# Kernel tuning notes

Measured on AMD Instinct MI355X. Metric: run time of the kernel, lower is better.

Reference implementation:

```python
import jax, jax.numpy as jnp
import numpy as np

N_CODE, PC = 127, 63
LENGTH = N_CODE + PC          # 190
D_MODEL, D_STATE, D_CONV, EXPAND = 512, 16, 4, 2
D_INNER = EXPAND * D_MODEL    # 1024
DT_RANK = (D_MODEL + 15) // 16  # 32
BATCH = 16


def _build_mask(pcm):
    # faithful translation of build_mask(code)
    L = N_CODE + PC
    mask = np.eye(L, dtype=np.float64)
    for r in range(PC):
        idx = np.where(pcm[r] > 0)[0]
        for jj in idx:
            for kk in idx:
                if jj != kk:
                    mask[jj, kk] += 1
                    mask[kk, jj] += 1
                    mask[N_CODE + r, jj] += 1
                    mask[jj, N_CODE + r] += 1
    return mask > 0


def setup_inputs() -> dict:
    rng = np.random.default_rng(0)
    # LDPC-like sparse parity-check matrix, row weight 6
    pcm = np.zeros((PC, N_CODE), np.int32)
    for r in range(PC):
        pcm[r, rng.choice(N_CODE, 6, replace=False)] = 1
    pc_mask = jnp.asarray(_build_mask(pcm))

    def w(shape, fan_in):
        return jnp.asarray((rng.standard_normal(shape) / np.sqrt(fan_in)).astype(np.float32))

    inp = {
        "x": jnp.asarray(rng.standard_normal((BATCH, LENGTH, D_MODEL)).astype(np.float32)),
        "pc_mask": pc_mask,
        # masked resize linears (torch Linear: y = x @ W.T + b)
        "in_resize_w": w((LENGTH, D_MODEL), D_MODEL),
        "in_resize_b": jnp.zeros((LENGTH,), jnp.float32),
        "in_reset_w": w((D_MODEL, LENGTH), LENGTH),
        "in_reset_b": jnp.zeros((D_MODEL,), jnp.float32),
        "out_resize_w": w((LENGTH, D_MODEL), D_MODEL),
        "out_resize_b": jnp.zeros((LENGTH,), jnp.float32),
        "out_reset_w": w((D_MODEL, LENGTH), LENGTH),
        "out_reset_b": jnp.zeros((D_MODEL,), jnp.float32),
        # Mamba block params
        "in_proj_w": w((2 * D_INNER, D_MODEL), D_MODEL),
        "conv_w": w((D_INNER, D_CONV), D_CONV),          # depthwise conv kernels
        "conv_b": jnp.zeros((D_INNER,), jnp.float32),
        "x_proj_w": w((DT_RANK + 2 * D_STATE, D_INNER), D_INNER),
        "dt_proj_w": w((D_INNER, DT_RANK), DT_RANK),
        "dt_proj_b": jnp.full((D_INNER,), -4.6, jnp.float32),  # softplus ~ 0.01
        "A_log": jnp.log(jnp.tile(jnp.arange(1, D_STATE + 1, dtype=jnp.float32), (D_INNER, 1))),
        "D": jnp.ones((D_INNER,), jnp.float32),
        "out_proj_w": w((D_MODEL, D_INNER), D_INNER),
        # LayerNorm over (length, d_model)
        "norm_w": jnp.ones((LENGTH, D_MODEL), jnp.float32),
        "norm_b": jnp.zeros((LENGTH, D_MODEL), jnp.float32),
    }
    return inp


def _forward(x, pc_mask, in_resize_w, in_resize_b, in_reset_w, in_reset_b,
             out_resize_w, out_resize_b, out_reset_w, out_reset_b,
             in_proj_w, conv_w, conv_b, x_proj_w, dt_proj_w, dt_proj_b,
             A_log, D, out_proj_w, norm_w, norm_b):
    dt_rank = dt_proj_w.shape[1]
    d_state = A_log.shape[1]
    d_conv = conv_w.shape[1]

    def mamba(h):
        # h: [B, L, d_model]
        xz = h @ in_proj_w.T                       # [B, L, 2*d_inner]
        xc, z = jnp.split(xz, 2, axis=-1)
        # depthwise causal conv along L
        xt = xc.transpose(0, 2, 1)                 # [B, d_inner, L]
        xt = jax.lax.conv_general_dilated(
            xt, conv_w[:, None, :], (1,), [(d_conv - 1, 0)],
            dimension_numbers=("NCH", "OIH", "NCH"),
            feature_group_count=xt.shape[1])
        xc = jax.nn.silu((xt + conv_b[None, :, None]).transpose(0, 2, 1))  # [B,L,di]
        x_dbl = xc @ x_proj_w.T                    # [B, L, dt_rank+2*ds]
        dt = jax.nn.softplus(x_dbl[..., :dt_rank] @ dt_proj_w.T + dt_proj_b)
        Bm = x_dbl[..., dt_rank:dt_rank + d_state]  # [B, L, ds]
        Cm = x_dbl[..., dt_rank + d_state:]         # [B, L, ds]
        A = -jnp.exp(A_log)                         # [di, ds]
        dA = jnp.exp(dt[..., None] * A)             # [B, L, di, ds]
        dBu = (dt * xc)[..., None] * Bm[:, :, None, :]

        def step(hst, inp):
            a, b = inp
            hst = a * hst + b
            return hst, hst

        h0 = jnp.zeros((dA.shape[0], dA.shape[2], dA.shape[3]), dA.dtype)
        _, hs = jax.lax.scan(step, h0, (dA.transpose(1, 0, 2, 3), dBu.transpose(1, 0, 2, 3)))
        y = jnp.einsum("lbds,bls->bld", hs, Cm) + xc * D
        return (y * jax.nn.silu(z)) @ out_proj_w.T  # [B, L, d_model]

    m = pc_mask.astype(x.dtype)
    h = (x @ in_resize_w.T + in_resize_b) * m[0, 0]
    h = (h @ in_reset_w.T + in_reset_b) * x
    o = mamba(h) + jnp.flip(mamba(jnp.flip(h, 1)), 1)  # bidirectional scan
    o = (o @ out_resize_w.T + out_resize_b) * m        # [B,L,L] * [L,L]
    o = (o @ out_reset_w.T + out_reset_b) * x
    # LayerNorm over last two dims (length, d_model)
    t = jnp.tanh(x)
    mu = jnp.mean(t, axis=(-2, -1), keepdims=True)
    var = jnp.var(t, axis=(-2, -1), keepdims=True)
    out = (t - mu) * jax.lax.rsqrt(var + 1e-5) * norm_w + norm_b
    # original module returns only `out`; `o` is also returned here to keep the
    # (otherwise dead) bidirectional selective-scan path observable.
    return out, o


def reference(x, pc_mask, in_resize_w, in_resize_b, in_reset_w, in_reset_b,
              out_resize_w, out_resize_b, out_reset_w, out_reset_b,
              in_proj_w, conv_w, conv_b, x_proj_w, dt_proj_w, dt_proj_b,
              A_log, D, out_proj_w, norm_w, norm_b):
    return _forward(x, pc_mask, in_resize_w, in_resize_b, in_reset_w, in_reset_b,
                    out_resize_w, out_resize_b, out_reset_w, out_reset_b,
                    in_proj_w, conv_w, conv_b, x_proj_w, dt_proj_w, dt_proj_b,
                    A_log, D, out_proj_w, norm_w, norm_b)
```

## Files before the change

### kernel.cpp

```cpp
#include <hip/hip_runtime.h>
#include <hip/hip_bf16.h>

#define B_    16
#define L_    190
#define LP_   192
#define DM_   512
#define DI_   1024
#define LB_   3040
#define RT_   6080
#define LBDI_ 3112960

typedef __attribute__((ext_vector_type(8))) short bf16x8;
typedef __attribute__((ext_vector_type(4))) float f32x4;
typedef __attribute__((ext_vector_type(4))) unsigned short u16x4;

typedef const __attribute__((address_space(1))) void gvoid;
typedef __attribute__((address_space(3))) void lvoid;
#define LOAD_LDS16(g, l) __builtin_amdgcn_global_load_lds((gvoid*)(g), (lvoid*)(l), 16, 0, 0)

__device__ __forceinline__ float siluf(float v) { return v / (1.f + __expf(-v)); }
__device__ __forceinline__ float softplusf(float v) {
  return v > 0.f ? v + log1pf(__expf(-v)) : log1pf(__expf(v));
}
__device__ __forceinline__ float bf2f(unsigned short u) {
  unsigned int w = (unsigned int)u << 16; return __builtin_bit_cast(float, w);
}

__global__ __launch_bounds__(256) void mask_convert(const void* __restrict__ pcm,
                                                    float* __restrict__ maskf,
                                                    const float* __restrict__ irb,
                                                    const float* __restrict__ orb,
                                                    float* __restrict__ b_inrs,
                                                    float* __restrict__ b_outrs)
{
  __shared__ int votes[3];
  if (threadIdx.x < 3) votes[threadIdx.x] = 0;
  __syncthreads();
  if (threadIdx.x < 48) {
    int idx = threadIdx.x * 191;
    const unsigned char* p8  = (const unsigned char*)pcm;
    const unsigned int*  p32 = (const unsigned int*)pcm;
    if (p8[idx] == 1) atomicAdd(&votes[0], 1);
    unsigned int v = p32[idx];
    if (v == 1u)          atomicAdd(&votes[1], 1);
    if (v == 0x3f800000u) atomicAdd(&votes[2], 1);
  }
  __syncthreads();
  int mode = (votes[0] >= 48) ? 0 : (votes[1] >= 48 ? 1 : (votes[2] >= 48 ? 2 : 0));
  int i = blockIdx.x * 256 + threadIdx.x;
  if (i < L_ * LP_) {
    int r = i / LP_, c = i % LP_;
    float v = 0.f;
    if (c < L_) {
      int s = r * L_ + c;
      if (mode == 0)      v = ((const unsigned char*)pcm)[s] ? 1.f : 0.f;
      else if (mode == 1) v = ((const int*)pcm)[s] ? 1.f : 0.f;
      else                v = ((const float*)pcm)[s];
    }
    maskf[i] = v;
  }
  if (blockIdx.x == 0 && threadIdx.x < LP_) {
    b_inrs[threadIdx.x]  = (threadIdx.x < L_) ? irb[threadIdx.x] : 0.f;
    b_outrs[threadIdx.x] = (threadIdx.x < L_) ? orb[threadIdx.x] : 0.f;
  }
}

struct Cvt2 { const float* src; __hip_bfloat16* dst; int R, C, Rp, Cp; };
struct CvtPack2 { Cvt2 d[9]; };

__global__ __launch_bounds__(256) void cvt_all2(CvtPack2 p)
{
  Cvt2 D = p.d[blockIdx.y];
  int n = D.Rp * D.Cp;
  if (D.C == D.Cp) {
    int nsrc = D.R * D.C;
    for (int i4 = (blockIdx.x * 256 + threadIdx.x) * 4; i4 < n; i4 += gridDim.x * 256 * 4) {
      __hip_bfloat16 o[4];
      if (i4 + 3 < nsrc) {
        f32x4 v = *(const f32x4*)(D.src + i4);
        #pragma unroll
        for (int q = 0; q < 4; ++q) o[q] = __float2bfloat16(v[q]);
      } else {
        #pragma unroll
        for (int q = 0; q < 4; ++q) { int i = i4 + q; o[q] = __float2bfloat16(i < nsrc ? D.src[i] : 0.f); }
      }
      *(u16x4*)(D.dst + i4) = *(u16x4*)o;
    }
  } else {
    for (int i = blockIdx.x * 256 + threadIdx.x; i < n; i += gridDim.x * 256) {
      int r = i / D.Cp, c = i - r * D.Cp;
      float v = (r < D.R && c < D.C) ? D.src[(size_t)r * D.C + c] : 0.f;
      D.dst[i] = __float2bfloat16(v);
    }
  }
}

template<int EPI, bool OF32, bool OBF>
__global__ __launch_bounds__(256) void gemm128(
    const __hip_bfloat16* __restrict__ A, int lda, int M,
    const __hip_bfloat16* __restrict__ Bw, int Brows,
    const float* __restrict__ bias, const float* __restrict__ aux,
    float* __restrict__ Cf, __hip_bfloat16* __restrict__ Cb,
    int N, int K)
{
  __shared__ bf16x8 SA[2][512];
  __shared__ bf16x8 SB[2][512];
  const int tid = threadIdx.x;
  const int wave = tid >> 6, lane = tid & 63;
  const int m0 = blockIdx.y * 128, n0 = blockIdx.x * 128;
  const int wm = (wave >> 1) * 64, wn = (wave & 1) * 64;
  const int l15 = lane & 15, lkb = lane >> 4;

  f32x4 acc[4][4] = {};

  auto stage = [&](int bsel, int k0) {
    #pragma unroll
    for (int it = 0; it < 2; ++it) {
      int c = it * 256 + tid;
      int row = c & 127, kb = c >> 7;
      int ar = m0 + row; ar = ar < M ? ar : M - 1;
      const __hip_bfloat16* ga = A + (size_t)ar * lda + (k0 + kb * 8);
      LOAD_LDS16(ga, &SA[bsel][it * 256 + wave * 64]);
      int br = n0 + row; br = br < Brows ? br : Brows - 1;
      const __hip_bfloat16* gb = Bw + (size_t)br * K + (k0 + kb * 8);
      LOAD_LDS16(gb, &SB[bsel][it * 256 + wave * 64]);
    }
  };

  const int nk = K >> 5;
  stage(0, 0);
  __syncthreads();
  int buf = 0;
  for (int kt = 0; kt < nk; ++kt) {
    if (kt + 1 < nk) stage(buf ^ 1, (kt + 1) * 32);
    bf16x8 af[4], bq[4];
    #pragma unroll
    for (int f = 0; f < 4; ++f) {
      af[f] = SA[buf][lkb * 128 + wm + f * 16 + l15];
      bq[f] = SB[buf][lkb * 128 + wn + f * 16 + l15];
    }
    #pragma unroll
    for (int i = 0; i < 4; ++i)
      #pragma unroll
      for (int j = 0; j < 4; ++j)
        acc[i][j] = __builtin_amdgcn_mfma_f32_16x16x32_bf16(af[i], bq[j], acc[i][j], 0, 0, 0);
    __syncthreads();
    buf ^= 1;
  }

  #pragma unroll
  for (int i = 0; i < 4; ++i) {
    int r0 = m0 + wm + i * 16 + (lkb << 2);
    #pragma unroll
    for (int j = 0; j < 4; ++j) {
      int col = n0 + wn + j * 16 + l15;
      if (col >= N) continue;
      #pragma unroll
      for (int r = 0; r < 4; ++r) {
        int row = r0 + r;
        if (row >= M) continue;
        float v = acc[i][j][r];
        if (EPI >= 1) v += bias[col];
        if (EPI == 2) v *= aux[(size_t)row * N + col];
        if (EPI == 3) v = softplusf(v);
        if (EPI == 4) v *= aux[(size_t)(row % L_) * N + col];
        if (OF32) Cf[(size_t)row * N + col] = v;
        if (OBF)  Cb[(size_t)row * N + col] = __float2bfloat16(v);
      }
    }
  }
}

template<int EPI, bool OF32, bool OBF>
__global__ __launch_bounds__(256) void gemm64(
    const __hip_bfloat16* __restrict__ A, int lda, int M,
    const __hip_bfloat16* __restrict__ Bw, int Brows,
    const float* __restrict__ bias, const float* __restrict__ aux,
    float* __restrict__ Cf, __hip_bfloat16* __restrict__ Cb,
    int N, int K)
{
  __shared__ bf16x8 SA[2][256];
  __shared__ bf16x8 SB[2][256];
  const int tid = threadIdx.x;
  const int wave = tid >> 6, lane = tid & 63;
  const int m0 = blockIdx.y * 64, n0 = blockIdx.x * 64;
  const int wm = (wave >> 1) * 32, wn = (wave & 1) * 32;
  const int l15 = lane & 15, lkb = lane >> 4;

  f32x4 acc[2][2] = {};

  auto stage = [&](int bsel, int k0) {
    int row = tid & 63, kb = tid >> 6;
    int ar = m0 + row; ar = ar < M ? ar : M - 1;
    const __hip_bfloat16* ga = A + (size_t)ar * lda + (k0 + kb * 8);
    LOAD_LDS16(ga, &SA[bsel][wave * 64]);
    int br = n0 + row; br = br < Brows ? br : Brows - 1;
    const __hip_bfloat16* gb = Bw + (size_t)br * K + (k0 + kb * 8);
    LOAD_LDS16(gb, &SB[bsel][wave * 64]);
  };

  const int nk = K >> 5;
  stage(0, 0);
  __syncthreads();
  int buf = 0;
  for (int kt = 0; kt < nk; ++kt) {
    if (kt + 1 < nk) stage(buf ^ 1, (kt + 1) * 32);
    bf16x8 af[2], bq[2];
    #pragma unroll
    for (int f = 0; f < 2; ++f) {
      af[f] = SA[buf][lkb * 64 + wm + f * 16 + l15];
      bq[f] = SB[buf][lkb * 64 + wn + f * 16 + l15];
    }
    #pragma unroll
    for (int i = 0; i < 2; ++i)
      #pragma unroll
      for (int j = 0; j < 2; ++j)
        acc[i][j] = __builtin_amdgcn_mfma_f32_16x16x32_bf16(af[i], bq[j], acc[i][j], 0, 0, 0);
    __syncthreads();
    buf ^= 1;
  }

  #pragma unroll
  for (int i = 0; i < 2; ++i) {
    int r0 = m0 + wm + i * 16 + (lkb << 2);
    #pragma unroll
    for (int j = 0; j < 2; ++j) {
      int col = n0 + wn + j * 16 + l15;
      if (col >= N) continue;
      #pragma unroll
      for (int r = 0; r < 4; ++r) {
        int row = r0 + r;
        if (row >= M) continue;
        float v = acc[i][j][r];
        if (EPI >= 1) v += bias[col];
        if (EPI == 2) v *= aux[(size_t)row * N + col];
        if (EPI == 3) v = softplusf(v);
        if (EPI == 4) v *= aux[(size_t)(row % L_) * N + col];
        if (OF32) Cf[(size_t)row * N + col] = v;
        if (OBF)  Cb[(size_t)row * N + col] = __float2bfloat16(v);
      }
    }
  }
}

__global__ __launch_bounds__(256) void conv_silu(
    const __hip_bfloat16* __restrict__ xz, const float* __restrict__ w,
    const float* __restrict__ cb, __hip_bfloat16* __restrict__ xcbf)
{
  int t = blockIdx.x * 256 + threadIdx.x;
  int c4 = (t & (DI_ / 4 - 1)) * 4;
  int bl = t >> 8;
  int l = bl % L_;
  int b = bl / L_;
  const __hip_bfloat16* base = xz + (size_t)b * L_ * (2 * DI_) + c4;
  float xr[7][4];
  #pragma unroll
  for (int j = 0; j < 7; ++j) {
    int gl = l + j - 3;
    if (gl >= 0 && gl < L_) {
      u16x4 v = *(const u16x4*)(base + (size_t)gl * (2 * DI_));
      #pragma unroll
      for (int q = 0; q < 4; ++q) xr[j][q] = bf2f(v[q]);
    } else {
      #pragma unroll
      for (int q = 0; q < 4; ++q) xr[j][q] = 0.f;
    }
  }
  __hip_bfloat16 of[4], ob[4];
  #pragma unroll
  for (int q = 0; q < 4; ++q) {
    int c = c4 + q;
    float w0 = w[c * 4], w1 = w[c * 4 + 1], w2 = w[c * 4 + 2], w3 = w[c * 4 + 3];
    float bias = cb[c];
    float sf = fmaf(w0, xr[0][q], fmaf(w1, xr[1][q], fmaf(w2, xr[2][q], fmaf(w3, xr[3][q], bias))));
    float sb = fmaf(w0, xr[6][q], fmaf(w1, xr[5][q], fmaf(w2, xr[4][q], fmaf(w3, xr[3][q], bias))));
    of[q] = __float2bfloat16(siluf(sf));
    ob[q] = __float2bfloat16(siluf(sb));
  }
  size_t o = (size_t)bl * DI_ + c4;
  *(u16x4*)(xcbf + o)         = *(u16x4*)of;
  *(u16x4*)(xcbf + LBDI_ + o) = *(u16x4*)ob;
}

#define CT_  12
#define BCS_ 33
#define HS_  17
__global__ __launch_bounds__(256) void scan_v6(
    const __hip_bfloat16* __restrict__ dtb,
    const float* __restrict__ xd,
    const __hip_bfloat16* __restrict__ xc,
    const float* __restrict__ A_log, const float* __restrict__ Dv,
    __hip_bfloat16* __restrict__ y)
{
  __shared__ float sBC[L_ * BCS_];
  __shared__ float sH[256 * HS_];
  __shared__ float sS[256];

  const int tid   = threadIdx.x;
  const int dl    = tid & 15;
  const int chunk = tid >> 4;
  const int dglob = blockIdx.x * 16 + dl;
  const int b     = blockIdx.y;
  const int dir   = blockIdx.z;
  const int rowbase = dir * LB_ + b * L_;
  const unsigned short* xcu = (const unsigned short*)xc;
  const unsigned short* dtu = (const unsigned short*)dtb;
  const float* Arow = A_log + dglob * 16;

  const float* xr = xd + (size_t)rowbase * 64;
  for (int i = tid; i < L_ * 8; i += 256) {
    int row = i >> 3, q = i & 7;
    f32x4 v = *(const f32x4*)(xr + (size_t)row * 64 + 32 + q * 4);
    *(f32x4*)(sBC + row * BCS_ + q * 4) = v;
  }

  const float A0 = -__expf(Arow[0]);
  bool fast = true;
  #pragma unroll
  for (int s = 1; s < 16; ++s) {
    float As = -__expf(Arow[s]);
    fast = fast && (fabsf(As - (float)(s + 1) * A0) <= 1e-4f * (float)(s + 1));
  }
  const float Dd = Dv[dglob];

  const int cstart = chunk * CT_;
  const int clen = (cstart + CT_ <= L_) ? CT_ : (L_ > cstart ? L_ - cstart : 0);

  __syncthreads();

  float h[16];
  #pragma unroll
  for (int s = 0; s < 16; ++s) h[s] = 0.f;
  float dsum = 0.f;
  for (int k = 0; k < clen; ++k) {
    int l   = cstart + k;
    int pos = dir ? (L_ - 1 - l) : l;
    size_t grow = (size_t)(rowbase + pos);
    float dtv = bf2f(dtu[grow * DI_ + dglob]);
    float xcv = bf2f(xcu[grow * DI_ + dglob]);
    float du  = dtv * xcv;
    dsum += dtv;
    const float* brow = sBC + pos * BCS_;
    f32x4 bq0 = *(const f32x4*)(brow + 0);
    f32x4 bq1 = *(const f32x4*)(brow + 4);
    f32x4 bq2 = *(const f32x4*)(brow + 8);
    f32x4 bq3 = *(const f32x4*)(brow + 12);
    float ep[16];
    if (fast) {
      float e1 = __expf(dtv * A0);
      float e = e1;
      #pragma unroll
      for (int s = 0; s < 16; ++s) { ep[s] = e; e *= e1; }
    } else {
      #pragma unroll
      for (int s = 0; s < 16; ++s) ep[s] = __expf(dtv * -__expf(Arow[s]));
    }
    #pragma unroll
    for (int s = 0; s < 16; ++s) {
      float Bv = (s < 4) ? bq0[s & 3] : (s < 8) ? bq1[s & 3] : (s < 12) ? bq2[s & 3] : bq3[s & 3];
      h[s] = fmaf(ep[s], h[s], du * Bv);
    }
  }
  {
    float* hr = sH + tid * HS_;
    #pragma unroll
    for (int s = 0; s < 16; ++s) hr[s] = h[s];
    sS[tid] = dsum;
  }
  __syncthreads();

  float hin[16];
  #pragma unroll
  for (int s = 0; s < 16; ++s) hin[s] = 0.f;
  for (int c = 0; c < chunk; ++c) {
    float S = sS[c * 16 + dl];
    const float* hp = sH + (c * 16 + dl) * HS_;
    float ep[16];
    if (fast) {
      float e1 = __expf(A0 * S);
      float e = e1;
      #pragma unroll
      for (int s = 0; s < 16; ++s) { ep[s] = e; e *= e1; }
    } else {
      #pragma unroll
      for (int s = 0; s < 16; ++s) ep[s] = __expf(-__expf(Arow[s]) * S);
    }
    #pragma unroll
    for (int s = 0; s < 16; ++s)
      hin[s] = fmaf(ep[s], hin[s], hp[s]);
  }

  #pragma unroll
  for (int s = 0; s < 16; ++s) h[s] = hin[s];
  for (int k = 0; k < clen; ++k) {
    int l   = cstart + k;
    int pos = dir ? (L_ - 1 - l) : l;
    size_t grow = (size_t)(rowbase + pos);
    float dtv = bf2f(dtu[grow * DI_ + dglob]);
    float xcv = bf2f(xcu[grow * DI_ + dglob]);
    float du  = dtv * xcv;
    const float* brow = sBC + pos * BCS_;
    f32x4 bq0 = *(const f32x4*)(brow + 0);
    f32x4 bq1 = *(const f32x4*)(brow + 4);
    f32x4 bq2 = *(const f32x4*)(brow + 8);
    f32x4 bq3 = *(const f32x4*)(brow + 12);
    f32x4 cq0 = *(const f32x4*)(brow + 16);
    f32x4 cq1 = *(const f32x4*)(brow + 20);
    f32x4 cq2 = *(const f32x4*)(brow + 24);
    f32x4 cq3 = *(const f32x4*)(brow + 28);
    float ep[16];
    if (fast) {
      float e1 = __expf(dtv * A0);
      float e = e1;
      #pragma unroll
      for (int s = 0; s < 16; ++s) { ep[s] = e; e *= e1; }
    } else {
      #pragma unroll
      for (int s = 0; s < 16; ++s) ep[s] = __expf(dtv * -__expf(Arow[s]));
    }
    float acc = 0.f;
    #pragma unroll
    for (int s = 0; s < 16; ++s) {
      float Bv = (s < 4) ? bq0[s & 3] : (s < 8) ? bq1[s & 3] : (s < 12) ? bq2[s & 3] : bq3[s & 3];
      float Cv = (s < 4) ? cq0[s & 3] : (s < 8) ? cq1[s & 3] : (s < 12) ? cq2[s & 3] : cq3[s & 3];
      h[s] = fmaf(ep[s], h[s], du * Bv);
      acc  = fmaf(h[s], Cv, acc);
    }
    y[grow * DI_ + dglob] = __float2bfloat16(fmaf(xcv, Dd, acc));
  }
}

__global__ __launch_bounds__(256) void combine_yz(
    const __hip_bfloat16* __restrict__ y, const __hip_bfloat16* __restrict__ xz,
    __hip_bfloat16* __restrict__ yz)
{
  int t = blockIdx.x * 256 + threadIdx.x;
  int c4 = (t & (DI_ / 4 - 1)) * 4;
  int rowi = t >> 8;
  size_t o = (size_t)rowi * DI_ + c4;
  u16x4 yf = *(const u16x4*)(y + o);
  u16x4 yb = *(const u16x4*)(y + LBDI_ + o);
  u16x4 zv = *(const u16x4*)(xz + (size_t)rowi * (2 * DI_) + DI_ + c4);
  __hip_bfloat16 out[4];
  #pragma unroll
  for (int q = 0; q < 4; ++q) {
    float z = bf2f(zv[q]);
    out[q] = __float2bfloat16((bf2f(yf[q]) + bf2f(yb[q])) * siluf(z));
  }
  *(u16x4*)(yz + o) = *(u16x4*)out;
}

__global__ __launch_bounds__(256) void ln_partial(const float* __restrict__ x,
                                                  float* __restrict__ partials)
{
  int b = blockIdx.y, ch = blockIdx.x;
  const float* xb = x + (size_t)b * (L_ * DM_);
  int lo = ch * 12160, hi = lo + 12160;
  float s = 0.f, s2 = 0.f;
  for (int i = lo + threadIdx.x; i < hi; i += 256) {
    float t = tanhf(xb[i]);
    s += t; s2 = fmaf(t, t, s2);
  }
  #pragma unroll
  for (int off = 32; off > 0; off >>= 1) { s += __shfl_down(s, off); s2 += __shfl_down(s2, off); }
  __shared__ float rs[4], rs2[4];
  int wid = threadIdx.x >> 6, lane = threadIdx.x & 63;
  if (lane == 0) { rs[wid] = s; rs2[wid] = s2; }
  __syncthreads();
  if (threadIdx.x == 0) {
    partials[(b * 8 + ch) * 2 + 0] = rs[0] + rs[1] + rs[2] + rs[3];
    partials[(b * 8 + ch) * 2 + 1] = rs2[0] + rs2[1] + rs2[2] + rs2[3];
  }
}

__global__ __launch_bounds__(256) void ln_final(const float* __restrict__ x,
    const float* __restrict__ partials,
    const float* __restrict__ nw, const float* __restrict__ nb,
    float* __restrict__ out)
{
  int b = blockIdx.y, ch = blockIdx.x;
  float S = 0.f, S2 = 0.f;
  #pragma unroll
  for (int i = 0; i < 8; ++i) { S += partials[(b * 8 + i) * 2 + 0]; S2 += partials[(b * 8 + i) * 2 + 1]; }
  const float inv = 1.f / (float)(L_ * DM_);
  float mu = S * inv;
  float var = S2 * inv - mu * mu;
  float r = rsqrtf(var + 1e-5f);
  const float* xb = x + (size_t)b * (L_ * DM_);
  float* ob = out + (size_t)b * (L_ * DM_);
  int lo = ch * 12160, hi = lo + 12160;
  for (int i = lo + threadIdx.x; i < hi; i += 256) {
    float t = tanhf(xb[i]);
    ob[i] = fmaf((t - mu) * r, nw[i], nb[i]);
  }
}

extern "C" void kernel_launch(void* const* d_in, const int* in_sizes, int n_in,
                              void* d_out, int out_size, void* d_ws, size_t ws_size,
                              hipStream_t stream)
{
  const float* x            = (const float*)d_in[0];
  const void*  pc_mask      = d_in[1];
  const float* in_resize_w  = (const float*)d_in[2];
  const float* in_resize_b  = (const float*)d_in[3];
  const float* in_reset_w   = (const float*)d_in[4];
  const float* in_reset_b   = (const float*)d_in[5];
  const float* out_resize_w = (const float*)d_in[6];
  const float* out_resize_b = (const float*)d_in[7];
  const float* out_reset_w  = (const float*)d_in[8];
  const float* out_reset_b  = (const float*)d_in[9];
  const float* in_proj_w    = (const float*)d_in[10];
  const float* conv_w       = (const float*)d_in[11];
  const float* conv_b       = (const float*)d_in[12];
  const float* x_proj_w     = (const float*)d_in[13];
  const float* dt_proj_w    = (const float*)d_in[14];
  const float* dt_proj_b    = (const float*)d_in[15];
  const float* A_log        = (const float*)d_in[16];
  const float* Dv           = (const float*)d_in[17];
  const float* out_proj_w   = (const float*)d_in[18];
  const float* norm_w       = (const float*)d_in[19];
  const float* norm_b       = (const float*)d_in[20];

  float* W = (float*)d_ws;
  float* maskf    = W + 0;
  float* b_inrs   = W + 36480;
  float* b_outrs  = W + 36672;
  float* xd       = W + 36864;
  float* partials = W + 425984;
  __hip_bfloat16* BF = (__hip_bfloat16*)(W + 426240);
  __hip_bfloat16* w_inrs  = BF + 0;
  __hip_bfloat16* w_inrt  = BF + 98304;
  __hip_bfloat16* w_inpj  = BF + 196608;
  __hip_bfloat16* w_xpj   = BF + 1245184;
  __hip_bfloat16* w_dtpj  = BF + 1310720;
  __hip_bfloat16* w_outpj = BF + 1343488;
  __hip_bfloat16* w_outrs = BF + 1867776;
  __hip_bfloat16* w_outrt = BF + 1966080;
  __hip_bfloat16* x_bf    = BF + 2064384;
  __hip_bfloat16* h1_bf   = BF + 3620864;
  __hip_bfloat16* h_bf    = BF + 4204544;
  __hip_bfloat16* xz_bf   = BF + 5761024;
  __hip_bfloat16* xc_bf   = BF + 11986944;
  __hip_bfloat16* y_bf    = BF + 18212864;
  __hip_bfloat16* xd_bf   = BF + 24438784;
  __hip_bfloat16* dt_bf   = BF + 24827904;
  __hip_bfloat16* yz_bf   = BF + 31053824;
  __hip_bfloat16* o_pre   = BF + 34166784;
  __hip_bfloat16* o2_bf   = BF + 35723264;

  float* out_ln = (float*)d_out;
  float* out_o  = (float*)d_out + (size_t)LB_ * DM_;

  dim3 blk(256);

  mask_convert<<<dim3(143), blk, 0, stream>>>(pc_mask, maskf, in_resize_b, out_resize_b, b_inrs, b_outrs);

  CvtPack2 P;
  P.d[0] = Cvt2{ x,            x_bf,    3040, 512, 3040, 512 };
  P.d[1] = Cvt2{ in_resize_w,  w_inrs,  190, 512, 192, 512 };
  P.d[2] = Cvt2{ in_reset_w,   w_inrt,  512, 190, 512, 192 };
  P.d[3] = Cvt2{ in_proj_w,    w_inpj,  2048, 512, 2048, 512 };
  P.d[4] = Cvt2{ x_proj_w,     w_xpj,   64, 1024, 64, 1024 };
  P.d[5] = Cvt2{ dt_proj_w,    w_dtpj,  1024, 32, 1024, 32 };
  P.d[6] = Cvt2{ out_proj_w,   w_outpj, 512, 1024, 512, 1024 };
  P.d[7] = Cvt2{ out_resize_w, w_outrs, 190, 512, 192, 512 };
  P.d[8] = Cvt2{ out_reset_w,  w_outrt, 512, 190, 512, 192 };
  cvt_all2<<<dim3(256, 9), blk, 0, stream>>>(P);

  gemm64<1,false,true><<<dim3(3,48), blk, 0, stream>>>(x_bf, 512, 3040, w_inrs, 192, b_inrs, nullptr, nullptr, h1_bf, LP_, 512);
  gemm64<2,false,true><<<dim3(8,48), blk, 0, stream>>>(h1_bf, LP_, 3040, w_inrt, 512, in_reset_b, x, nullptr, h_bf, 512, LP_);
  gemm128<0,false,true><<<dim3(16,24), blk, 0, stream>>>(h_bf, 512, 3040, w_inpj, 2048, nullptr, nullptr, nullptr, xz_bf, 2048, 512);
  conv_silu<<<dim3(LBDI_/1024), blk, 0, stream>>>(xz_bf, conv_w, conv_b, xc_bf);
  gemm64<0,true,true><<<dim3(1,95), blk, 0, stream>>>(xc_bf, 1024, 6080, w_xpj, 64, nullptr, nullptr, xd, xd_bf, 64, 1024);
  gemm64<3,false,true><<<dim3(16,95), blk, 0, stream>>>(xd_bf, 64, 6080, w_dtpj, 1024, dt_proj_b, nullptr, nullptr, dt_bf, 1024, 32);
  scan_v6<<<dim3(64, 16, 2), blk, 0, stream>>>(dt_bf, xd, xc_bf, A_log, Dv, y_bf);
  combine_yz<<<dim3(LBDI_/1024), blk, 0, stream>>>(y_bf, xz_bf, yz_bf);
  gemm64<0,false,true><<<dim3(8,48), blk, 0, stream>>>(yz_bf, 1024, 3040, w_outpj, 512, nullptr, nullptr, nullptr, o_pre, 512, 1024);
  gemm64<4,false,true><<<dim3(3,48), blk, 0, stream>>>(o_pre, 512, 3040, w_outrs, 192, b_outrs, maskf, nullptr, o2_bf, LP_, 512);
  gemm64<2,true,false><<<dim3(8,48), blk, 0, stream>>>(o2_bf, LP_, 3040, w_outrt, 512, out_reset_b, x, out_o, nullptr, 512, LP_);
  dim3 lgrid(8, B_);
  ln_partial<<<lgrid, blk, 0, stream>>>(x, partials);
  ln_final<<<lgrid, blk, 0, stream>>>(x, partials, norm_w, norm_b, out_ln);
}
```

Before: 317.0 us.

## Restructure chunked selective scan into single pass with carry-in output correction

After: 855.8 us. 2.7x slower.

```diff
diff --git a/kernel.cpp b/kernel.cpp
--- a/kernel.cpp
+++ b/kernel.cpp
@@ -282,10 +282,10 @@
   *(u16x4*)(xcbf + LBDI_ + o) = *(u16x4*)ob;
 }
 
-#define CT_  12
+#define SCT_ 24
 #define BCS_ 33
 #define HS_  17
-__global__ __launch_bounds__(256) void scan_v6(
+__global__ __launch_bounds__(256) void scan_v7(
     const __hip_bfloat16* __restrict__ dtb,
     const float* __restrict__ xd,
     const __hip_bfloat16* __restrict__ xc,
@@ -297,9 +297,9 @@
   __shared__ float sS[256];
 
   const int tid   = threadIdx.x;
-  const int dl    = tid & 15;
-  const int chunk = tid >> 4;
-  const int dglob = blockIdx.x * 16 + dl;
+  const int dl    = tid & 31;
+  const int chunk = tid >> 5;
+  const int dglob = blockIdx.x * 32 + dl;
   const int b     = blockIdx.y;
   const int dir   = blockIdx.z;
   const int rowbase = dir * LB_ + b * L_;
@@ -322,83 +322,27 @@
     fast = fast && (fabsf(As - (float)(s + 1) * A0) <= 1e-4f * (float)(s + 1));
   }
   const float Dd = Dv[dglob];
-
-  const int cstart = chunk * CT_;
-  const int clen = (cstart + CT_ <= L_) ? CT_ : (L_ > cstart ? L_ - cstart : 0);
+  const int cstart = chunk * SCT_;
 
   __syncthreads();
 
   float h[16];
   #pragma unroll
   for (int s = 0; s < 16; ++s) h[s] = 0.f;
-  float dsum = 0.f;
-  for (int k = 0; k < clen; ++k) {
-    int l   = cstart + k;
+  float cum = 0.f;
+  float cumv[SCT_], yloc[SCT_];
+  #pragma unroll
+  for (int k = 0; k < SCT_; ++k) {
+    int l = cstart + k;
+    bool valid = l < L_;
     int pos = dir ? (L_ - 1 - l) : l;
+    pos = valid ? pos : 0;
     size_t grow = (size_t)(rowbase + pos);
-    float dtv = bf2f(dtu[grow * DI_ + dglob]);
-    float xcv = bf2f(xcu[grow * DI_ + dglob]);
-    float du  = dtv * xcv;
-    dsum += dtv;
-    const float* brow = sBC + pos * BCS_;
-    f32x4 bq0 = *(const f32x4*)(brow + 0);
-    f32x4 bq1 = *(const f32x4*)(brow + 4);
-    f32x4 bq2 = *(const f32x4*)(brow + 8);
-    f32x4 bq3 = *(const f32x4*)(brow + 12);
-    float ep[16];
-    if (fast) {
-      float e1 = __expf(dtv * A0);
-      float e = e1;
-      #pragma unroll
-      for (int s = 0; s < 16; ++s) { ep[s] = e; e *= e1; }
-    } else {
-      #pragma unroll
-      for (int s = 0; s < 16; ++s) ep[s] = __expf(dtv * -__expf(Arow[s]));
-    }
-    #pragma unroll
-    for (int s = 0; s < 16; ++s) {
-      float Bv = (s < 4) ? bq0[s & 3] : (s < 8) ? bq1[s & 3] : (s < 12) ? bq2[s & 3] : bq3[s & 3];
-      h[s] = fmaf(ep[s], h[s], du * Bv);
-    }
-  }
-  {
-    float* hr = sH + tid * HS_;
-    #pragma unroll
-    for (int s = 0; s < 16; ++s) hr[s] = h[s];
-    sS[tid] = dsum;
-  }
-  __syncthreads();
-
-  float hin[16];
-  #pragma unroll
-  for (int s = 0; s < 16; ++s) hin[s] = 0.f;
-  for (int c = 0; c < chunk; ++c) {
-    float S = sS[c * 16 + dl];
-    const float* hp = sH + (c * 16 + dl) * HS_;
-    float ep[16];
-    if (fast) {
-      float e1 = __expf(A0 * S);
-      float e = e1;
-      #pragma unroll
-      for (int s = 0; s < 16; ++s) { ep[s] = e; e *= e1; }
-    } else {
-      #pragma unroll
-      for (int s = 0; s < 16; ++s) ep[s] = __expf(-__expf(Arow[s]) * S);
-    }
-    #pragma unroll
-    for (int s = 0; s < 16; ++s)
-      hin[s] = fmaf(ep[s], hin[s], hp[s]);
-  }
-
-  #pragma unroll
-  for (int s = 0; s < 16; ++s) h[s] = hin[s];
-  for (int k = 0; k < clen; ++k) {
-    int l   = cstart + k;
-    int pos = dir ? (L_ - 1 - l) : l;
-    size_t grow = (size_t)(rowbase + pos);
-    float dtv = bf2f(dtu[grow * DI_ + dglob]);
-    float xcv = bf2f(xcu[grow * DI_ + dglob]);
-    float du  = dtv * xcv;
+    float dtv = valid ? bf2f(dtu[grow * DI_ + dglob]) : 0.f;
+    float xcv = valid ? bf2f(xcu[grow * DI_ + dglob]) : 0.f;
+    cum += dtv;
+    cumv[k] = cum;
+    float du = dtv * xcv;
     const float* brow = sBC + pos * BCS_;
     f32x4 bq0 = *(const f32x4*)(brow + 0);
     f32x4 bq1 = *(const f32x4*)(brow + 4);
@@ -426,7 +370,76 @@
       h[s] = fmaf(ep[s], h[s], du * Bv);
       acc  = fmaf(h[s], Cv, acc);
     }
-    y[grow * DI_ + dglob] = __float2bfloat16(fmaf(xcv, Dd, acc));
+    yloc[k] = fmaf(xcv, Dd, acc);
+  }
+  {
+    float* hr = sH + tid * HS_;
+    #pragma unroll
+    for (int s = 0; s < 16; ++s) hr[s] = h[s];
+    sS[tid] = cum;
+  }
+  __syncthreads();
+
+  #pragma unroll
+  for (int s = 0; s < 16; ++s) h[s] = 0.f;
+  for (int c = 0; c < chunk; ++c) {
+    float S = sS[c * 32 + dl];
+    const float* hp = sH + (c * 32 + dl) * HS_;
+    float ep[16];
+    if (fast) {
+      float e1 = __expf(A0 * S);
+      float e = e1;
+      #pragma unroll
+      for (int s = 0; s < 16; ++s) { ep[s] = e; e *= e1; }
+    } else {
+      #pragma unroll
+      for (int s = 0; s < 16; ++s) ep[s] = __expf(-__expf(Arow[s]) * S);
+    }
+    #pragma unroll
+    for (int s = 0; s < 16; ++s)
+      h[s] = fmaf(ep[s], h[s], hp[s]);
+  }
+
+  if (chunk == 0) {
+    #pragma unroll
+    for (int k = 0; k < SCT_; ++k) {
+      int l = cstart + k;
+      if (l < L_) {
+        int pos = dir ? (L_ - 1 - l) : l;
+        y[(size_t)(rowbase + pos) * DI_ + dglob] = __float2bfloat16(yloc[k]);
+      }
+    }
+  } else {
+    #pragma unroll
+    for (int k = 0; k < SCT_; ++k) {
+      int l = cstart + k;
+      bool valid = l < L_;
+      int pos = dir ? (L_ - 1 - l) : l;
+      pos = valid ? pos : 0;
+      const float* brow = sBC + pos * BCS_;
+      f32x4 cq0 = *(const f32x4*)(brow + 16);
+      f32x4 cq1 = *(const f32x4*)(brow + 20);
+      f32x4 cq2 = *(const f32x4*)(brow + 24);
+      f32x4 cq3 = *(const f32x4*)(brow + 28);
+      float ep[16];
+      if (fast) {
+        float e1 = __expf(A0 * cumv[k]);
+        float e = e1;
+        #pragma unroll
+        for (int s = 0; s < 16; ++s) { ep[s] = e; e *= e1; }
+      } else {
+        #pragma unroll
+        for (int s = 0; s < 16; ++s) ep[s] = __expf(-__expf(Arow[s]) * cumv[k]);
+      }
+      float corr = 0.f;
+      #pragma unroll
+      for (int s = 0; s < 16; ++s) {
+        float Cv = (s < 4) ? cq0[s & 3] : (s < 8) ? cq1[s & 3] : (s < 12) ? cq2[s & 3] : cq3[s & 3];
+        corr = fmaf(Cv * ep[s], h[s], corr);
+      }
+      if (valid)
+        y[(size_t)(rowbase + pos) * DI_ + dglob] = __float2bfloat16(yloc[k] + corr);
+    }
   }
 }
 
@@ -573,7 +586,7 @@
   conv_silu<<<dim3(LBDI_/1024), blk, 0, stream>>>(xz_bf, conv_w, conv_b, xc_bf);
   gemm64<0,true,true><<<dim3(1,95), blk, 0, stream>>>(xc_bf, 1024, 6080, w_xpj, 64, nullptr, nullptr, xd, xd_bf, 64, 1024);
   gemm64<3,false,true><<<dim3(16,95), blk, 0, stream>>>(xd_bf, 64, 6080, w_dtpj, 1024, dt_proj_b, nullptr, nullptr, dt_bf, 1024, 32);
-  scan_v6<<<dim3(64, 16, 2), blk, 0, stream>>>(dt_bf, xd, xc_bf, A_log, Dv, y_bf);
+  scan_v7<<<dim3(32, 16, 2), blk, 0, stream>>>(dt_bf, xd, xc_bf, A_log, Dv, y_bf);
   combine_yz<<<dim3(LBDI_/1024), blk, 0, stream>>>(y_bf, xz_bf, yz_bf);
   gemm64<0,false,true><<<dim3(8,48), blk, 0, stream>>>(yz_bf, 1024, 3040, w_outpj, 512, nullptr, nullptr, nullptr, o_pre, 512, 1024);
   gemm64<4,false,true><<<dim3(3,48), blk, 0, stream>>>(o_pre, 512, 3040, w_outrs, 192, b_outrs, maskf, nullptr, o2_bf, LP_, 512);
```
